# Performance work log

Hardware: AMD Instinct MI355X
Metric: run time of the kernel (lower is better)

## Reference

```python
import jax, jax.numpy as jnp
import numpy as np

INPUT_DIM = 512
HIDDEN_DIM = 512


def setup_inputs() -> dict:
    key = jax.random.key(0)
    ks = jax.random.split(key, 17)
    B, T = 64, 1024
    x_seq = jax.random.normal(ks[0], (B, T, INPUT_DIM), dtype=jnp.float32)
    s_h = 1.0 / np.sqrt(HIDDEN_DIM)
    s_x = 1.0 / np.sqrt(INPUT_DIM)
    inp = {"x_seq": x_seq}
    names = ["hf", "xf", "hi", "xi", "hg", "xg", "ho", "xo"]
    for i, nm in enumerate(names):
        in_dim = HIDDEN_DIM if nm[0] == "h" else INPUT_DIM
        s = s_h if nm[0] == "h" else s_x
        inp[f"W_{nm}"] = jax.random.uniform(ks[1 + 2 * i], (HIDDEN_DIM, in_dim), minval=-s, maxval=s, dtype=jnp.float32)
        inp[f"b_{nm}"] = jax.random.uniform(ks[2 + 2 * i], (HIDDEN_DIM,), minval=-s, maxval=s, dtype=jnp.float32)
    return inp


def reference(x_seq, W_hf, b_hf, W_xf, b_xf, W_hi, b_hi, W_xi, b_xi,
              W_hg, b_hg, W_xg, b_xg, W_ho, b_ho, W_xo, b_xo):
    B, T, _ = x_seq.shape
    H = W_hf.shape[0]
    # Precompute input projections for all timesteps: [B,T,4H]
    Wx = jnp.concatenate([W_xf, W_xi, W_xg, W_xo], axis=0)  # [4H, D_in]
    bx = jnp.concatenate([b_xf, b_xi, b_xg, b_xo], axis=0)
    Wh = jnp.concatenate([W_hf, W_hi, W_hg, W_ho], axis=0)  # [4H, H]
    bh = jnp.concatenate([b_hf, b_hi, b_hg, b_ho], axis=0)
    x_proj = jnp.einsum('btd,gd->btg', x_seq, Wx) + bx  # [B,T,4H]

    def step(carry, xp_t):
        h, c = carry
        gates = xp_t + h @ Wh.T + bh  # [B,4H]
        f = jax.nn.sigmoid(gates[:, 0:H])
        i = jax.nn.sigmoid(gates[:, H:2 * H])
        g = jnp.tanh(gates[:, 2 * H:3 * H])
        o = jax.nn.sigmoid(gates[:, 3 * H:4 * H])
        c_new = f * c + i * g
        h_new = o * jnp.tanh(c_new)
        return (h_new, c_new), None

    h0 = jnp.zeros((B, H), dtype=x_seq.dtype)
    c0 = jnp.zeros((B, H), dtype=x_seq.dtype)
    (h_final, _), _ = jax.lax.scan(step, (h0, c0), jnp.swapaxes(x_proj, 0, 1))
    return h_final
```

## Files before the change

kernel.cpp:

```cpp
#include <hip/hip_runtime.h>
#include <cstdint>
#include <cstddef>


typedef _Float16 half8  __attribute__((ext_vector_type(8)));
typedef _Float16 half4v __attribute__((ext_vector_type(4)));
typedef float    float4v __attribute__((ext_vector_type(4)));

__device__ __forceinline__ float sigm(float x) { return 1.f / (1.f + __expf(-x)); }
__device__ __forceinline__ float tanh_f(float x) { return 2.f / (1.f + __expf(-2.f * x)) - 1.f; }

__global__ __launch_bounds__(256) void xcvt(const float* __restrict__ X,
                                            _Float16* __restrict__ XH) {
    size_t i = ((size_t)blockIdx.x * 256 + threadIdx.x) * 8;
    float4 a = *(const float4*)(X + i);
    float4 b = *(const float4*)(X + i + 4);
    half8 v;
    v[0] = (_Float16)a.x; v[1] = (_Float16)a.y; v[2] = (_Float16)a.z; v[3] = (_Float16)a.w;
    v[4] = (_Float16)b.x; v[5] = (_Float16)b.y; v[6] = (_Float16)b.z; v[7] = (_Float16)b.w;
    *(half8*)(XH + i) = v;
}

__global__ __launch_bounds__(256, 1) void lstm_rec(
    const float* __restrict__ Whf, const float* __restrict__ Whi,
    const float* __restrict__ Whg, const float* __restrict__ Who,
    const float* __restrict__ Wxf, const float* __restrict__ Wxi,
    const float* __restrict__ Wxg, const float* __restrict__ Wxo,
    const float* __restrict__ bxf, const float* __restrict__ bxi,
    const float* __restrict__ bxg, const float* __restrict__ bxo,
    const float* __restrict__ bhf, const float* __restrict__ bhi,
    const float* __restrict__ bhg, const float* __restrict__ bho,
    const _Float16* __restrict__ XH,
    unsigned long long* __restrict__ hws,
    float* __restrict__ out)
{
    const int blk  = blockIdx.x;
    const int g    = blk & 7;
    const int c    = blk >> 3;
    const int tid  = threadIdx.x;
    const int w    = tid >> 6;
    const int lane = tid & 63;
    const int l15  = lane & 15;
    const int quad = lane >> 4;
    const int m    = l15 & 7;

    __shared__ _Float16 Wls[64][520];
    __shared__ _Float16 Xls[64][520];
    __shared__ _Float16 hls[8][520];
    __shared__ float    gs[8][65];

    const float* WhSeg[4] = {Whf, Whi, Whg, Who};
    const float* WxSeg[4] = {Wxf, Wxi, Wxg, Wxo};
    for (int e = tid * 4; e < 64 * 512; e += 1024) {
        int row = e >> 9, col = e & 511;
        int seg = row >> 4;
        int srow = c * 16 + (row & 15);
        float4 vh = *(const float4*)(WhSeg[seg] + (size_t)srow * 512 + col);
        float4 vx = *(const float4*)(WxSeg[seg] + (size_t)srow * 512 + col);
        half4v th = {(_Float16)vh.x, (_Float16)vh.y, (_Float16)vh.z, (_Float16)vh.w};
        half4v tx = {(_Float16)vx.x, (_Float16)vx.y, (_Float16)vx.z, (_Float16)vx.w};
        *(half4v*)&Wls[row][col] = th;
        *(half4v*)&Xls[row][col] = tx;
    }
    __syncthreads();

    const int erow = tid >> 3;
    const int ep   = tid & 7;
    float bs[8] = {0.f};
    if (tid < 64) {
        int u0 = c * 16 + 2 * ep, u1 = u0 + 1;
        bs[0] = bxf[u0] + bhf[u0];  bs[4] = bxf[u1] + bhf[u1];
        bs[1] = bxi[u0] + bhi[u0];  bs[5] = bxi[u1] + bhi[u1];
        bs[2] = bxg[u0] + bhg[u0];  bs[6] = bxg[u1] + bhg[u1];
        bs[3] = bxo[u0] + bho[u0];  bs[7] = bxo[u1] + bho[u1];
    }
    float c0s = 0.f, c1s = 0.f;

    const int crow = tid >> 5;
    const int ccol = (tid & 31) << 4;

    const size_t xrow = (size_t)(g * 8 + m) * 1024 * 512 + (size_t)quad * 8;
    half8 xf[16];
#pragma unroll
    for (int kk = 0; kk < 16; kk++) xf[kk] = *(const half8*)(XH + xrow + kk * 32);
    float4v accx = {0.f, 0.f, 0.f, 0.f};
#pragma unroll
    for (int kk = 0; kk < 16; kk++) {
        half8 b = *(const half8*)&Xls[w * 16 + l15][kk * 32 + quad * 8];
        accx = __builtin_amdgcn_mfma_f32_16x16x32_f16(xf[kk], b, accx, 0, 0, 0);
    }

    for (int t = 0; t < 1024; t++) {
        {
            const unsigned long long* hsrc = hws + (size_t)(t & 1) * 16384
                                           + (size_t)g * 2048 + (size_t)tid * 8;
            const unsigned long long T =
                ((unsigned long long)(unsigned)t << 16) |
                ((unsigned long long)(unsigned)t << 48);
            unsigned long long q[8];
            for (;;) {
                unsigned long long bad = 0;
#pragma unroll
                for (int j = 0; j < 8; j++)
                    q[j] = __hip_atomic_load(hsrc + j, __ATOMIC_RELAXED,
                                             __HIP_MEMORY_SCOPE_AGENT);
#pragma unroll
                for (int j = 0; j < 8; j++)
                    bad |= (q[j] ^ T) & 0xFFFF0000FFFF0000ULL;
                if (!bad) break;
            }
            unsigned int* hd = (unsigned int*)&hls[crow][ccol];
#pragma unroll
            for (int j = 0; j < 8; j++)
                hd[j] = (unsigned int)(q[j] & 0xFFFF) |
                        (((unsigned int)(q[j] >> 32)) << 16);
        }
        __syncthreads();

        float4v acca = accx;
        float4v accb = {0.f, 0.f, 0.f, 0.f};
#pragma unroll
        for (int kk = 0; kk < 16; kk += 2) {
            half8 a0 = *(const half8*)&hls[m][kk * 32 + quad * 8];
            half8 a1 = *(const half8*)&hls[m][(kk + 1) * 32 + quad * 8];
            half8 b0 = *(const half8*)&Wls[w * 16 + l15][kk * 32 + quad * 8];
            half8 b1 = *(const half8*)&Wls[w * 16 + l15][(kk + 1) * 32 + quad * 8];
            acca = __builtin_amdgcn_mfma_f32_16x16x32_f16(a0, b0, acca, 0, 0, 0);
            accb = __builtin_amdgcn_mfma_f32_16x16x32_f16(a1, b1, accb, 0, 0, 0);
        }

        if (quad < 2) {
#pragma unroll
            for (int r = 0; r < 4; r++)
                gs[quad * 4 + r][w * 16 + l15] = acca[r] + accb[r];
        }
        __syncthreads();

        if (tid < 64) {
            float pf0 = gs[erow][2 * ep]      + bs[0];
            float pi0 = gs[erow][2 * ep + 16] + bs[1];
            float pg0 = gs[erow][2 * ep + 32] + bs[2];
            float po0 = gs[erow][2 * ep + 48] + bs[3];
            float pf1 = gs[erow][2 * ep + 1]  + bs[4];
            float pi1 = gs[erow][2 * ep + 17] + bs[5];
            float pg1 = gs[erow][2 * ep + 33] + bs[6];
            float po1 = gs[erow][2 * ep + 49] + bs[7];
            c0s = sigm(pf0) * c0s + sigm(pi0) * tanh_f(pg0);
            c1s = sigm(pf1) * c1s + sigm(pi1) * tanh_f(pg1);
            float hn0 = sigm(po0) * tanh_f(c0s);
            float hn1 = sigm(po1) * tanh_f(c1s);
            union { _Float16 f; unsigned short u; } cv0, cv1;
            cv0.f = (_Float16)hn0; cv1.f = (_Float16)hn1;
            unsigned int tag = (unsigned)(t + 1) << 16;
            unsigned long long qv = (unsigned long long)(tag | cv0.u)
                                  | ((unsigned long long)(tag | cv1.u) << 32);
            unsigned long long* hd = hws + (size_t)((t + 1) & 1) * 16384
                                   + (size_t)g * 2048 + (size_t)erow * 256
                                   + c * 8 + ep;
            __hip_atomic_store(hd, qv, __ATOMIC_RELAXED,
                               __HIP_MEMORY_SCOPE_AGENT);
            if (t == 1023) {
                size_t ob = (size_t)(g * 8 + erow) * 512 + c * 16 + 2 * ep;
                out[ob]     = hn0;
                out[ob + 1] = hn1;
            }
        }

        int tn = (t < 1023) ? (t + 1) : 0;
        const _Float16* xp = XH + xrow + (size_t)tn * 512;
#pragma unroll
        for (int kk = 0; kk < 16; kk++) xf[kk] = *(const half8*)(xp + kk * 32);
        float4v ax = {0.f, 0.f, 0.f, 0.f};
#pragma unroll
        for (int kk = 0; kk < 16; kk++) {
            half8 b = *(const half8*)&Xls[w * 16 + l15][kk * 32 + quad * 8];
            ax = __builtin_amdgcn_mfma_f32_16x16x32_f16(xf[kk], b, ax, 0, 0, 0);
        }
        accx = ax;
    }
}

extern "C" void kernel_launch(void* const* d_in, const int* in_sizes, int n_in,
                              void* d_out, int out_size, void* d_ws, size_t ws_size,
                              hipStream_t stream) {
    const float* X   = (const float*)d_in[0];
    const float* Whf = (const float*)d_in[1];  const float* bhf = (const float*)d_in[2];
    const float* Wxf = (const float*)d_in[3];  const float* bxf = (const float*)d_in[4];
    const float* Whi = (const float*)d_in[5];  const float* bhi = (const float*)d_in[6];
    const float* Wxi = (const float*)d_in[7];  const float* bxi = (const float*)d_in[8];
    const float* Whg = (const float*)d_in[9];  const float* bhg = (const float*)d_in[10];
    const float* Wxg = (const float*)d_in[11]; const float* bxg = (const float*)d_in[12];
    const float* Who = (const float*)d_in[13]; const float* bho = (const float*)d_in[14];
    const float* Wxo = (const float*)d_in[15]; const float* bxo = (const float*)d_in[16];

    if (ws_size < (size_t)68157440) return;

    char* ws = (char*)d_ws;
    unsigned long long* hws = (unsigned long long*)ws;
    _Float16*           XH  = (_Float16*)(ws + (1 << 20));
    (void)in_sizes; (void)n_in; (void)out_size;

    hipMemsetAsync(d_ws, 0, 262144, stream);
    xcvt<<<16384, 256, 0, stream>>>(X, XH);
    lstm_rec<<<256, 256, 0, stream>>>(Whf, Whi, Whg, Who, Wxf, Wxi, Wxg, Wxo,
                                      bxf, bxi, bxg, bxo, bhf, bhi, bhg, bho,
                                      XH, hws, (float*)d_out);
}
```

Measured before the change: 4.019 ms.

## Interleave gate rows and compute LSTM cell via lane shuffles, drop shared-memory barrier

Reorders the gate weight rows so each group of four adjacent MFMA output columns holds the f,i,g,o gates of one hidden unit. The cell update then runs in registers using wavefront shuffles, which removes the gs shared buffer, one __syncthreads per timestep, and the single-wave serial activation stage. The h exchange layout is changed so each thread issues wide dwordx4 burst loads and dwordx2 stores through inline asm with sc0/sc1 cache bypass bits. This shortens the per-step critical path of the cross-block recurrence, at the cost of redundant activation math in non-publishing lanes and reliance on hand-written memory-ordering semantics.

```diff
diff --git a/kernel.cpp b/kernel.cpp
--- a/kernel.cpp
+++ b/kernel.cpp
@@ -6,9 +6,25 @@
 typedef _Float16 half8  __attribute__((ext_vector_type(8)));
 typedef _Float16 half4v __attribute__((ext_vector_type(4)));
 typedef float    float4v __attribute__((ext_vector_type(4)));
+typedef unsigned int uint4v __attribute__((ext_vector_type(4)));
 
 __device__ __forceinline__ float sigm(float x) { return 1.f / (1.f + __expf(-x)); }
 __device__ __forceinline__ float tanh_f(float x) { return 2.f / (1.f + __expf(-2.f * x)) - 1.f; }
+
+__device__ __forceinline__ void st_u64(unsigned long long* p, unsigned long long v) {
+    asm volatile("global_store_dwordx2 %0, %1, off sc0 sc1" :: "v"(p), "v"(v) : "memory");
+}
+
+__device__ __forceinline__ void ld_burst64(const void* p, uint4v q[4]) {
+    asm volatile(
+        "global_load_dwordx4 %[a], %[p], off sc0 sc1\n\t"
+        "global_load_dwordx4 %[b], %[p], off offset:16 sc0 sc1\n\t"
+        "global_load_dwordx4 %[c], %[p], off offset:32 sc0 sc1\n\t"
+        "global_load_dwordx4 %[d], %[p], off offset:48 sc0 sc1\n\t"
+        "s_waitcnt vmcnt(0)"
+        : [a]"=&v"(q[0]), [b]"=&v"(q[1]), [c]"=&v"(q[2]), [d]"=&v"(q[3])
+        : [p]"v"(p) : "memory");
+}
 
 __global__ __launch_bounds__(256) void xcvt(const float* __restrict__ X,
                                             _Float16* __restrict__ XH) {
@@ -47,16 +63,15 @@
     __shared__ _Float16 Wls[64][520];
     __shared__ _Float16 Xls[64][520];
     __shared__ _Float16 hls[8][520];
-    __shared__ float    gs[8][65];
 
     const float* WhSeg[4] = {Whf, Whi, Whg, Who};
     const float* WxSeg[4] = {Wxf, Wxi, Wxg, Wxo};
     for (int e = tid * 4; e < 64 * 512; e += 1024) {
         int row = e >> 9, col = e & 511;
-        int seg = row >> 4;
-        int srow = c * 16 + (row & 15);
-        float4 vh = *(const float4*)(WhSeg[seg] + (size_t)srow * 512 + col);
-        float4 vx = *(const float4*)(WxSeg[seg] + (size_t)srow * 512 + col);
+        int gate = row & 3;
+        int srow = c * 16 + ((row >> 4) << 2) + ((row >> 2) & 3);
+        float4 vh = *(const float4*)(WhSeg[gate] + (size_t)srow * 512 + col);
+        float4 vx = *(const float4*)(WxSeg[gate] + (size_t)srow * 512 + col);
         half4v th = {(_Float16)vh.x, (_Float16)vh.y, (_Float16)vh.z, (_Float16)vh.w};
         half4v tx = {(_Float16)vx.x, (_Float16)vx.y, (_Float16)vx.z, (_Float16)vx.w};
         *(half4v*)&Wls[row][col] = th;
@@ -64,20 +79,19 @@
     }
     __syncthreads();
 
-    const int erow = tid >> 3;
-    const int ep   = tid & 7;
-    float bs[8] = {0.f};
-    if (tid < 64) {
-        int u0 = c * 16 + 2 * ep, u1 = u0 + 1;
-        bs[0] = bxf[u0] + bhf[u0];  bs[4] = bxf[u1] + bhf[u1];
-        bs[1] = bxi[u0] + bhi[u0];  bs[5] = bxi[u1] + bhi[u1];
-        bs[2] = bxg[u0] + bhg[u0];  bs[6] = bxg[u1] + bhg[u1];
-        bs[3] = bxo[u0] + bho[u0];  bs[7] = bxo[u1] + bho[u1];
-    }
-    float c0s = 0.f, c1s = 0.f;
-
-    const int crow = tid >> 5;
-    const int ccol = (tid & 31) << 4;
+    const int gate = l15 & 3;
+    const int unit = c * 16 + w * 4 + (l15 >> 2);
+    float bias;
+    {
+        float bx = (gate == 0) ? bxf[unit] : (gate == 1) ? bxi[unit]
+                 : (gate == 2) ? bxg[unit] : bxo[unit];
+        float bh = (gate == 0) ? bhf[unit] : (gate == 1) ? bhi[unit]
+                 : (gate == 2) ? bhg[unit] : bho[unit];
+        bias = bx + bh;
+    }
+    float cst[4] = {0.f, 0.f, 0.f, 0.f};
+    const int pub = ((l15 & 3) == 0) && (quad < 2);
+    const int base = lane & ~3;
 
     const size_t xrow = (size_t)(g * 8 + m) * 1024 * 512 + (size_t)quad * 8;
     half8 xf[16];
@@ -94,26 +108,27 @@
         {
             const unsigned long long* hsrc = hws + (size_t)(t & 1) * 16384
                                            + (size_t)g * 2048 + (size_t)tid * 8;
-            const unsigned long long T =
-                ((unsigned long long)(unsigned)t << 16) |
-                ((unsigned long long)(unsigned)t << 48);
-            unsigned long long q[8];
+            const unsigned int T = (unsigned)t << 16;
+            uint4v q[4];
             for (;;) {
-                unsigned long long bad = 0;
-#pragma unroll
-                for (int j = 0; j < 8; j++)
-                    q[j] = __hip_atomic_load(hsrc + j, __ATOMIC_RELAXED,
-                                             __HIP_MEMORY_SCOPE_AGENT);
-#pragma unroll
-                for (int j = 0; j < 8; j++)
-                    bad |= (q[j] ^ T) & 0xFFFF0000FFFF0000ULL;
+                ld_burst64(hsrc, q);
+                unsigned int bad = 0;
+#pragma unroll
+                for (int j = 0; j < 4; j++)
+#pragma unroll
+                    for (int e = 0; e < 4; e++)
+                        bad |= (q[j][e] ^ T) & 0xFFFF0000u;
                 if (!bad) break;
             }
-            unsigned int* hd = (unsigned int*)&hls[crow][ccol];
-#pragma unroll
-            for (int j = 0; j < 8; j++)
-                hd[j] = (unsigned int)(q[j] & 0xFFFF) |
-                        (((unsigned int)(q[j] >> 32)) << 16);
+#pragma unroll
+            for (int rp = 0; rp < 4; rp++) {
+                unsigned a_lo = q[(2 * rp) >> 2][(2 * rp) & 3];
+                unsigned a_hi = q[(2 * rp + 1) >> 2][(2 * rp + 1) & 3];
+                unsigned b_lo = q[(8 + 2 * rp) >> 2][(8 + 2 * rp) & 3];
+                unsigned b_hi = q[(9 + 2 * rp) >> 2][(9 + 2 * rp) & 3];
+                *(unsigned*)&hls[2 * rp][2 * tid]     = (a_lo & 0xFFFFu) | (b_lo << 16);
+                *(unsigned*)&hls[2 * rp + 1][2 * tid] = (a_hi & 0xFFFFu) | (b_hi << 16);
+            }
         }
         __syncthreads();
 
@@ -129,40 +144,36 @@
             accb = __builtin_amdgcn_mfma_f32_16x16x32_f16(a1, b1, accb, 0, 0, 0);
         }
 
-        if (quad < 2) {
-#pragma unroll
-            for (int r = 0; r < 4; r++)
-                gs[quad * 4 + r][w * 16 + l15] = acca[r] + accb[r];
-        }
-        __syncthreads();
-
-        if (tid < 64) {
-            float pf0 = gs[erow][2 * ep]      + bs[0];
-            float pi0 = gs[erow][2 * ep + 16] + bs[1];
-            float pg0 = gs[erow][2 * ep + 32] + bs[2];
-            float po0 = gs[erow][2 * ep + 48] + bs[3];
-            float pf1 = gs[erow][2 * ep + 1]  + bs[4];
-            float pi1 = gs[erow][2 * ep + 17] + bs[5];
-            float pg1 = gs[erow][2 * ep + 33] + bs[6];
-            float po1 = gs[erow][2 * ep + 49] + bs[7];
-            c0s = sigm(pf0) * c0s + sigm(pi0) * tanh_f(pg0);
-            c1s = sigm(pf1) * c1s + sigm(pi1) * tanh_f(pg1);
-            float hn0 = sigm(po0) * tanh_f(c0s);
-            float hn1 = sigm(po1) * tanh_f(c1s);
-            union { _Float16 f; unsigned short u; } cv0, cv1;
-            cv0.f = (_Float16)hn0; cv1.f = (_Float16)hn1;
-            unsigned int tag = (unsigned)(t + 1) << 16;
-            unsigned long long qv = (unsigned long long)(tag | cv0.u)
-                                  | ((unsigned long long)(tag | cv1.u) << 32);
-            unsigned long long* hd = hws + (size_t)((t + 1) & 1) * 16384
-                                   + (size_t)g * 2048 + (size_t)erow * 256
-                                   + c * 8 + ep;
-            __hip_atomic_store(hd, qv, __ATOMIC_RELAXED,
-                               __HIP_MEMORY_SCOPE_AGENT);
+        float hn[4];
+#pragma unroll
+        for (int r = 0; r < 4; r++) {
+            float pre = acca[r] + accb[r] + bias;
+            float fv = __shfl(pre, base + 0, 64);
+            float iv = __shfl(pre, base + 1, 64);
+            float gv = __shfl(pre, base + 2, 64);
+            float ov = __shfl(pre, base + 3, 64);
+            cst[r] = sigm(fv) * cst[r] + sigm(iv) * tanh_f(gv);
+            hn[r]  = sigm(ov) * tanh_f(cst[r]);
+        }
+
+        if (pub) {
+            unsigned tag = (unsigned)(t + 1) << 16;
+            union { _Float16 f; unsigned short u; } v0, v1, v2, v3;
+            v0.f = (_Float16)hn[0]; v1.f = (_Float16)hn[1];
+            v2.f = (_Float16)hn[2]; v3.f = (_Float16)hn[3];
+            unsigned long long q0 = (unsigned long long)(tag | v0.u)
+                                  | ((unsigned long long)(tag | v1.u) << 32);
+            unsigned long long q1 = (unsigned long long)(tag | v2.u)
+                                  | ((unsigned long long)(tag | v3.u) << 32);
+            unsigned long long* dst = hws + (size_t)((t + 1) & 1) * 16384
+                                    + (size_t)g * 2048 + (size_t)unit * 4
+                                    + (size_t)quad * 2;
+            st_u64(dst, q0);
+            st_u64(dst + 1, q1);
             if (t == 1023) {
-                size_t ob = (size_t)(g * 8 + erow) * 512 + c * 16 + 2 * ep;
-                out[ob]     = hn0;
-                out[ob + 1] = hn1;
+#pragma unroll
+                for (int r = 0; r < 4; r++)
+                    out[(size_t)(g * 8 + quad * 4 + r) * 512 + unit] = hn[r];
             }
         }
 
```

Measured after the change: 4.419 ms. 1.1x slower.
